# Kernel tuning notes

Hardware: AMD Instinct MI355X
Metric: run time of the kernel (lower is better)

## Reference

```python
import jax, jax.numpy as jnp
import numpy as np
from jax import lax

B, T, C = 4, 2048, 1024
E, DFF, TOPK = 8, 4096, 2


def setup_inputs() -> dict:
    key = jax.random.key(0)
    ks = jax.random.split(key, 5)
    scale = 0.02
    x = jax.random.normal(ks[0], (B, T, C), dtype=jnp.float32)
    router_w = jax.random.normal(ks[1], (C, E), dtype=jnp.float32) * scale
    router_b = jnp.zeros((E,), dtype=jnp.float32)
    w1 = jax.random.normal(ks[2], (E, C, DFF), dtype=jnp.float32) * scale
    b1 = jnp.zeros((E, DFF), dtype=jnp.float32)
    w2 = jax.random.normal(ks[3], (E, DFF, C), dtype=jnp.float32) * scale
    b2 = jnp.zeros((E, C), dtype=jnp.float32)
    return {"x": x, "router_w": router_w, "router_b": router_b,
            "w1": w1, "b1": b1, "w2": w2, "b2": b2, "top_k": TOPK}


def reference(x, router_w, router_b, w1, b1, w2, b2, top_k):
    # Router: softmax then top-k (matches torch.topk(F.softmax(logits)))
    logits = jnp.einsum('btc,ce->bte', x, router_w) + router_b   # [B,T,E]
    probs = jax.nn.softmax(logits, axis=-1)
    weights, indices = lax.top_k(probs, top_k)                    # [B,T,k]
    n_exp = w1.shape[0]
    # Combined per-expert weight per token (sum over top-k slots hitting expert j)
    onehot = jax.nn.one_hot(indices, n_exp, dtype=x.dtype)        # [B,T,k,E]
    cw = jnp.sum(weights[..., None] * onehot, axis=-2)            # [B,T,E]
    bsz, seq, dim = x.shape
    flat_x = x.reshape(-1, dim)                                   # [N,C]
    flat_cw = cw.reshape(-1, n_exp)                               # [N,E]
    out = jnp.zeros_like(flat_x)
    for j in range(n_exp):  # fixed small expert loop (dropout=0 -> eval)
        h = jax.nn.gelu(flat_x @ w1[j] + b1[j], approximate=False)
        out = out + flat_cw[:, j:j + 1] * (h @ w2[j] + b2[j])
    return out.reshape(bsz, seq, dim)
```

## Files before the change

kernel.cpp:

```cpp
#include <hip/hip_runtime.h>
#include <math.h>

typedef __bf16 bf16;
typedef bf16 bf16x4 __attribute__((ext_vector_type(4)));
typedef bf16 bf16x8 __attribute__((ext_vector_type(8)));
typedef float f32x4 __attribute__((ext_vector_type(4)));

#define NTOK 8192
#define CDIM 1024
#define EXP 8
#define DFF 4096
#define BM 128
#define BN 128
#define BK 32

__device__ __forceinline__ void gld_lds16(const bf16* g, bf16* l) {
  __builtin_amdgcn_global_load_lds(
      (const __attribute__((address_space(1))) unsigned int*)g,
      (__attribute__((address_space(3))) unsigned int*)l, 16, 0, 0);
}

__global__ __launch_bounds__(256) void convert_x(const float* __restrict__ in,
                                                 bf16* __restrict__ out) {
  int idx = (blockIdx.x * 256 + threadIdx.x) * 8;
  float4 a = *(const float4*)(in + idx);
  float4 b = *(const float4*)(in + idx + 4);
  bf16x8 v;
  v[0] = (bf16)a.x; v[1] = (bf16)a.y; v[2] = (bf16)a.z; v[3] = (bf16)a.w;
  v[4] = (bf16)b.x; v[5] = (bf16)b.y; v[6] = (bf16)b.z; v[7] = (bf16)b.w;
  *(bf16x8*)(out + idx) = v;
}

__global__ __launch_bounds__(256) void transpose_cvt(
    const float* __restrict__ in, bf16* __restrict__ out, int R, int Cin) {
  __shared__ float tile[32][33];
  int e = blockIdx.z;
  const float* ip = in + (size_t)e * R * Cin;
  bf16* op = out + (size_t)e * R * Cin;
  int c0 = blockIdx.x * 32, r0 = blockIdx.y * 32;
  int tx = threadIdx.x & 31, ty = threadIdx.x >> 5;
#pragma unroll
  for (int i = 0; i < 4; i++)
    tile[ty + 8 * i][tx] = ip[(size_t)(r0 + ty + 8 * i) * Cin + c0 + tx];
  __syncthreads();
  int c = threadIdx.x >> 3, r4 = (threadIdx.x & 7) * 4;
  bf16x4 v;
  v[0] = (bf16)tile[r4][c];
  v[1] = (bf16)tile[r4 + 1][c];
  v[2] = (bf16)tile[r4 + 2][c];
  v[3] = (bf16)tile[r4 + 3][c];
  *(bf16x4*)&op[(size_t)(c0 + c) * R + r0 + r4] = v;
}

__global__ __launch_bounds__(256) void router_kernel(
    const float* __restrict__ x, const float* __restrict__ rw,
    const float* __restrict__ rb, unsigned int* __restrict__ cnt,
    int* __restrict__ list, float* __restrict__ wq) {
  int wave = threadIdx.x >> 6, lane = threadIdx.x & 63;
  int t = blockIdx.x * 4 + wave;
  if (t >= NTOK) return;
  const float* xr = x + (size_t)t * CDIM;
  float acc[8] = {0.f, 0.f, 0.f, 0.f, 0.f, 0.f, 0.f, 0.f};
  for (int c = lane; c < CDIM; c += 64) {
    float xv = xr[c];
    const float4* rp = (const float4*)(rw + c * 8);
    float4 r0 = rp[0], r1 = rp[1];
    acc[0] += xv * r0.x; acc[1] += xv * r0.y;
    acc[2] += xv * r0.z; acc[3] += xv * r0.w;
    acc[4] += xv * r1.x; acc[5] += xv * r1.y;
    acc[6] += xv * r1.z; acc[7] += xv * r1.w;
  }
#pragma unroll
  for (int e = 0; e < 8; e++)
#pragma unroll
    for (int off = 32; off; off >>= 1) acc[e] += __shfl_down(acc[e], off);
  if (lane == 0) {
    float p[8], mx = -1e30f;
#pragma unroll
    for (int e = 0; e < 8; e++) { p[e] = acc[e] + rb[e]; mx = fmaxf(mx, p[e]); }
    float s = 0.f;
#pragma unroll
    for (int e = 0; e < 8; e++) { p[e] = expf(p[e] - mx); s += p[e]; }
    float inv = 1.0f / s;
#pragma unroll
    for (int e = 0; e < 8; e++) p[e] *= inv;
    int i1 = 0;
#pragma unroll
    for (int e = 1; e < 8; e++) if (p[e] > p[i1]) i1 = e;
    int i2 = (i1 == 0) ? 1 : 0;
#pragma unroll
    for (int e = 0; e < 8; e++) if (e != i1 && p[e] > p[i2]) i2 = e;
    unsigned s0 = atomicAdd(&cnt[i1], 1u);
    list[i1 * NTOK + s0] = t * 2;
    unsigned s1 = atomicAdd(&cnt[i2], 1u);
    list[i2 * NTOK + s1] = t * 2 + 1;
    wq[t * 2] = p[i1];
    wq[t * 2 + 1] = p[i2];
  }
}

__global__ __launch_bounds__(256) void gemm1_kernel(
    const bf16* __restrict__ xb, const bf16* __restrict__ w1b,
    const float* __restrict__ b1, const int* __restrict__ list,
    const unsigned int* __restrict__ cnt, bf16* __restrict__ h) {
  int e = blockIdx.z;
  int count = (int)min(cnt[e], (unsigned)NTOK);
  int m0 = blockIdx.y * BM;
  if (m0 >= count) return;
  int n0 = blockIdx.x * BN;

  __shared__ __align__(16) bf16 As[BM][BK];
  __shared__ __align__(16) bf16 Bs[BN][BK];
  __shared__ int Ls[BM];

  int tid = threadIdx.x;
  if (tid < BM) {
    int gi = m0 + tid;
    Ls[tid] = (gi < count) ? list[e * NTOK + gi] : 0;
  }
  __syncthreads();

  const bf16* arow0 = xb + (size_t)(Ls[tid >> 2] >> 1) * CDIM + (tid & 3) * 8;
  const bf16* arow1 =
      xb + (size_t)(Ls[64 + (tid >> 2)] >> 1) * CDIM + (tid & 3) * 8;
  bf16* adst0 = &As[tid >> 2][(tid & 3) * 8];
  bf16* adst1 = &As[64 + (tid >> 2)][(tid & 3) * 8];
  const bf16* brow0 = w1b + (size_t)e * DFF * CDIM +
                      (size_t)(n0 + (tid >> 2)) * CDIM + (tid & 3) * 8;
  const bf16* brow1 = brow0 + (size_t)64 * CDIM;
  bf16* bdst0 = &Bs[tid >> 2][(tid & 3) * 8];
  bf16* bdst1 = &Bs[64 + (tid >> 2)][(tid & 3) * 8];

  f32x4 acc[4][4] = {};
  int wave = tid >> 6, lane = tid & 63;
  int wm = wave & 1, wn = wave >> 1;
  int ln = lane & 15, kq = lane >> 4;

  for (int k0 = 0; k0 < CDIM; k0 += BK) {
    __syncthreads();
    gld_lds16(arow0 + k0, adst0);
    gld_lds16(arow1 + k0, adst1);
    gld_lds16(brow0 + k0, bdst0);
    gld_lds16(brow1 + k0, bdst1);
    __syncthreads();
    bf16x8 af[4], bfr[4];
#pragma unroll
    for (int i = 0; i < 4; i++)
      af[i] = *(bf16x8*)&As[wm * 64 + i * 16 + ln][kq * 8];
#pragma unroll
    for (int j = 0; j < 4; j++)
      bfr[j] = *(bf16x8*)&Bs[wn * 64 + j * 16 + ln][kq * 8];
#pragma unroll
    for (int i = 0; i < 4; i++)
#pragma unroll
      for (int j = 0; j < 4; j++)
        acc[i][j] = __builtin_amdgcn_mfma_f32_16x16x32_bf16(af[i], bfr[j],
                                                            acc[i][j], 0, 0, 0);
  }
#pragma unroll
  for (int j = 0; j < 4; j++) {
    int n = n0 + wn * 64 + j * 16 + ln;
    float b1v = b1[e * DFF + n];
#pragma unroll
    for (int i = 0; i < 4; i++) {
#pragma unroll
      for (int r = 0; r < 4; r++) {
        int mrow = wm * 64 + i * 16 + kq * 4 + r;
        if (m0 + mrow < count) {
          int enc = Ls[mrow];
          float v = acc[i][j][r] + b1v;
          float g = 0.5f * v * (1.0f + erff(v * 0.70710678118654752f));
          h[(size_t)enc * DFF + n] = (bf16)g;
        }
      }
    }
  }
}

__global__ __launch_bounds__(256) void gemm2_kernel(
    const bf16* __restrict__ h, const bf16* __restrict__ w2b,
    const float* __restrict__ b2, const int* __restrict__ list,
    const unsigned int* __restrict__ cnt, const float* __restrict__ wq,
    float* __restrict__ out) {
  int e = blockIdx.z;
  int count = (int)min(cnt[e], (unsigned)NTOK);
  int m0 = blockIdx.y * BM;
  if (m0 >= count) return;
  int n0 = blockIdx.x * BN;

  __shared__ __align__(16) bf16 As[BM][BK];
  __shared__ __align__(16) bf16 Bs[BN][BK];
  __shared__ int Ls[BM];

  int tid = threadIdx.x;
  if (tid < BM) {
    int gi = m0 + tid;
    Ls[tid] = (gi < count) ? list[e * NTOK + gi] : 0;
  }
  __syncthreads();

  const bf16* arow0 = h + (size_t)Ls[tid >> 2] * DFF + (tid & 3) * 8;
  const bf16* arow1 = h + (size_t)Ls[64 + (tid >> 2)] * DFF + (tid & 3) * 8;
  bf16* adst0 = &As[tid >> 2][(tid & 3) * 8];
  bf16* adst1 = &As[64 + (tid >> 2)][(tid & 3) * 8];
  const bf16* brow0 = w2b + (size_t)e * CDIM * DFF +
                      (size_t)(n0 + (tid >> 2)) * DFF + (tid & 3) * 8;
  const bf16* brow1 = brow0 + (size_t)64 * DFF;
  bf16* bdst0 = &Bs[tid >> 2][(tid & 3) * 8];
  bf16* bdst1 = &Bs[64 + (tid >> 2)][(tid & 3) * 8];

  f32x4 acc[4][4] = {};
  int wave = tid >> 6, lane = tid & 63;
  int wm = wave & 1, wn = wave >> 1;
  int ln = lane & 15, kq = lane >> 4;

  for (int k0 = 0; k0 < DFF; k0 += BK) {
    __syncthreads();
    gld_lds16(arow0 + k0, adst0);
    gld_lds16(arow1 + k0, adst1);
    gld_lds16(brow0 + k0, bdst0);
    gld_lds16(brow1 + k0, bdst1);
    __syncthreads();
    bf16x8 af[4], bfr[4];
#pragma unroll
    for (int i = 0; i < 4; i++)
      af[i] = *(bf16x8*)&As[wm * 64 + i * 16 + ln][kq * 8];
#pragma unroll
    for (int j = 0; j < 4; j++)
      bfr[j] = *(bf16x8*)&Bs[wn * 64 + j * 16 + ln][kq * 8];
#pragma unroll
    for (int i = 0; i < 4; i++)
#pragma unroll
      for (int j = 0; j < 4; j++)
        acc[i][j] = __builtin_amdgcn_mfma_f32_16x16x32_bf16(af[i], bfr[j],
                                                            acc[i][j], 0, 0, 0);
  }
#pragma unroll
  for (int j = 0; j < 4; j++) {
    int n = n0 + wn * 64 + j * 16 + ln;
    float b2v = b2[e * CDIM + n];
#pragma unroll
    for (int i = 0; i < 4; i++) {
#pragma unroll
      for (int r = 0; r < 4; r++) {
        int mrow = wm * 64 + i * 16 + kq * 4 + r;
        if (m0 + mrow < count) {
          int enc = Ls[mrow];
          int t = enc >> 1;
          float w = wq[enc];
          atomicAdd(&out[(size_t)t * CDIM + n], w * (acc[i][j][r] + b2v));
        }
      }
    }
  }
}

extern "C" void kernel_launch(void* const* d_in, const int* in_sizes, int n_in,
                              void* d_out, int out_size, void* d_ws,
                              size_t ws_size, hipStream_t stream) {
  const float* x = (const float*)d_in[0];
  const float* rw = (const float*)d_in[1];
  const float* rb = (const float*)d_in[2];
  const float* w1 = (const float*)d_in[3];
  const float* b1 = (const float*)d_in[4];
  const float* w2 = (const float*)d_in[5];
  const float* b2 = (const float*)d_in[6];
  float* out = (float*)d_out;

  char* ws = (char*)d_ws;
  size_t o = 0;
  auto carve = [&](size_t bytes) {
    void* p = ws + o;
    o = (o + bytes + 255) & ~(size_t)255;
    return p;
  };
  bf16* w1b = (bf16*)carve((size_t)EXP * DFF * CDIM * 2);
  bf16* w2b = (bf16*)carve((size_t)EXP * DFF * CDIM * 2);
  bf16* h = (bf16*)carve((size_t)2 * NTOK * DFF * 2);
  bf16* xb = (bf16*)carve((size_t)NTOK * CDIM * 2);
  int* list = (int*)carve((size_t)EXP * NTOK * 4);
  float* wq = (float*)carve((size_t)2 * NTOK * 4);
  unsigned int* cnt = (unsigned int*)carve(64);

  hipMemsetAsync(out, 0, (size_t)out_size * sizeof(float), stream);
  hipMemsetAsync(cnt, 0, 64, stream);

  convert_x<<<NTOK * CDIM / (256 * 8), 256, 0, stream>>>(x, xb);
  transpose_cvt<<<dim3(DFF / 32, CDIM / 32, EXP), 256, 0, stream>>>(w1, w1b,
                                                                    CDIM, DFF);
  transpose_cvt<<<dim3(CDIM / 32, DFF / 32, EXP), 256, 0, stream>>>(w2, w2b,
                                                                    DFF, CDIM);
  router_kernel<<<NTOK / 4, 256, 0, stream>>>(x, rw, rb, cnt, list, wq);
  gemm1_kernel<<<dim3(DFF / BN, NTOK / BM, EXP), 256, 0, stream>>>(
      xb, w1b, b1, list, cnt, h);
  gemm2_kernel<<<dim3(CDIM / BN, NTOK / BM, EXP), 256, 0, stream>>>(
      h, w2b, b2, list, cnt, wq, out);
}
```

Before: 1.175 ms.

## Enlarge MoE GEMM tiles to 256x256x64 with swizzled LDS and block remapping

Both expert GEMMs move from 128x128x32 tiles with 256 threads to 256x256x64 tiles with 512 threads, so each wave computes a 128x64 sub-tile. Operand reuse per LDS load goes up. LDS columns are XOR-swizzled on both the load and read sides to avoid bank conflicts. Workgroup IDs are remapped in groups of 8 to improve cache locality across experts and tiles. Larger tiles waste more work on partially filled expert tiles, and the bigger accumulator raises register pressure, which can limit occupancy.

```diff
diff --git a/kernel.cpp b/kernel.cpp
--- a/kernel.cpp
+++ b/kernel.cpp
@@ -10,9 +10,9 @@
 #define CDIM 1024
 #define EXP 8
 #define DFF 4096
-#define BM 128
-#define BN 128
-#define BK 32
+#define BM 256
+#define BN 256
+#define BK 64
 
 __device__ __forceinline__ void gld_lds16(const bf16* g, bf16* l) {
   __builtin_amdgcn_global_load_lds(
@@ -99,157 +99,179 @@
   }
 }
 
-__global__ __launch_bounds__(256) void gemm1_kernel(
+__global__ __launch_bounds__(512, 2) void gemm1_kernel(
     const bf16* __restrict__ xb, const bf16* __restrict__ w1b,
     const float* __restrict__ b1, const int* __restrict__ list,
     const unsigned int* __restrict__ cnt, bf16* __restrict__ h) {
-  int e = blockIdx.z;
+  int bid = blockIdx.x + 16 * (blockIdx.y + 32 * blockIdx.z);
+  int wg = (bid & 7) * 512 + (bid >> 3);
+  int n0 = (wg & 15) * BN;
+  int mt = (wg >> 4) & 31;
+  int e = wg >> 9;
   int count = (int)min(cnt[e], (unsigned)NTOK);
-  int m0 = blockIdx.y * BM;
+  int m0 = mt * BM;
   if (m0 >= count) return;
-  int n0 = blockIdx.x * BN;
 
   __shared__ __align__(16) bf16 As[BM][BK];
   __shared__ __align__(16) bf16 Bs[BN][BK];
-  __shared__ int Ls[BM];
 
   int tid = threadIdx.x;
-  if (tid < BM) {
-    int gi = m0 + tid;
-    Ls[tid] = (gi < count) ? list[e * NTOK + gi] : 0;
-  }
-  __syncthreads();
-
-  const bf16* arow0 = xb + (size_t)(Ls[tid >> 2] >> 1) * CDIM + (tid & 3) * 8;
-  const bf16* arow1 =
-      xb + (size_t)(Ls[64 + (tid >> 2)] >> 1) * CDIM + (tid & 3) * 8;
-  bf16* adst0 = &As[tid >> 2][(tid & 3) * 8];
-  bf16* adst1 = &As[64 + (tid >> 2)][(tid & 3) * 8];
-  const bf16* brow0 = w1b + (size_t)e * DFF * CDIM +
-                      (size_t)(n0 + (tid >> 2)) * CDIM + (tid & 3) * 8;
-  const bf16* brow1 = brow0 + (size_t)64 * CDIM;
-  bf16* bdst0 = &Bs[tid >> 2][(tid & 3) * 8];
-  bf16* bdst1 = &Bs[64 + (tid >> 2)][(tid & 3) * 8];
-
-  f32x4 acc[4][4] = {};
-  int wave = tid >> 6, lane = tid & 63;
-  int wm = wave & 1, wn = wave >> 1;
-  int ln = lane & 15, kq = lane >> 4;
+  int w = tid >> 6, l = tid & 63;
+  int lhi = l >> 3, llo = l & 7;
+  int w8l = w * 8 + lhi;
+  int dst8 = llo * 8;
+  int sc8 = (llo ^ lhi) * 8;
+
+  const int* lp = list + e * NTOK;
+  const bf16* aptr[4];
+  const bf16* bptr[4];
+#pragma unroll
+  for (int p = 0; p < 4; p++) {
+    int row = p * 64 + w8l;
+    int enc = lp[min(m0 + row, count - 1)];
+    aptr[p] = xb + (size_t)(enc >> 1) * CDIM + sc8;
+    bptr[p] = w1b + (size_t)e * DFF * CDIM + (size_t)(n0 + row) * CDIM + sc8;
+  }
+
+  f32x4 acc[8][4] = {};
+  int wm = w >> 2, wn = w & 3;
+  int ln = l & 15, kq = l >> 4;
+  int rx = ln & 7;
 
   for (int k0 = 0; k0 < CDIM; k0 += BK) {
     __syncthreads();
-    gld_lds16(arow0 + k0, adst0);
-    gld_lds16(arow1 + k0, adst1);
-    gld_lds16(brow0 + k0, bdst0);
-    gld_lds16(brow1 + k0, bdst1);
+#pragma unroll
+    for (int p = 0; p < 4; p++) {
+      gld_lds16(aptr[p] + k0, &As[p * 64 + w8l][dst8]);
+      gld_lds16(bptr[p] + k0, &Bs[p * 64 + w8l][dst8]);
+    }
     __syncthreads();
-    bf16x8 af[4], bfr[4];
-#pragma unroll
-    for (int i = 0; i < 4; i++)
-      af[i] = *(bf16x8*)&As[wm * 64 + i * 16 + ln][kq * 8];
-#pragma unroll
-    for (int j = 0; j < 4; j++)
-      bfr[j] = *(bf16x8*)&Bs[wn * 64 + j * 16 + ln][kq * 8];
-#pragma unroll
-    for (int i = 0; i < 4; i++)
+#pragma unroll
+    for (int hh = 0; hh < 2; hh++) {
+      int co = ((hh * 4 + kq) ^ rx) * 8;
+      bf16x8 af[8], bfr[4];
 #pragma unroll
       for (int j = 0; j < 4; j++)
-        acc[i][j] = __builtin_amdgcn_mfma_f32_16x16x32_bf16(af[i], bfr[j],
-                                                            acc[i][j], 0, 0, 0);
-  }
-#pragma unroll
-  for (int j = 0; j < 4; j++) {
-    int n = n0 + wn * 64 + j * 16 + ln;
-    float b1v = b1[e * DFF + n];
-#pragma unroll
-    for (int i = 0; i < 4; i++) {
-#pragma unroll
-      for (int r = 0; r < 4; r++) {
-        int mrow = wm * 64 + i * 16 + kq * 4 + r;
-        if (m0 + mrow < count) {
-          int enc = Ls[mrow];
-          float v = acc[i][j][r] + b1v;
+        bfr[j] = *(bf16x8*)&Bs[wn * 64 + j * 16 + ln][co];
+#pragma unroll
+      for (int i = 0; i < 8; i++)
+        af[i] = *(bf16x8*)&As[wm * 128 + i * 16 + ln][co];
+#pragma unroll
+      for (int i = 0; i < 8; i++)
+#pragma unroll
+        for (int j = 0; j < 4; j++)
+          acc[i][j] = __builtin_amdgcn_mfma_f32_16x16x32_bf16(
+              af[i], bfr[j], acc[i][j], 0, 0, 0);
+    }
+  }
+
+  float b1f[4];
+#pragma unroll
+  for (int j = 0; j < 4; j++)
+    b1f[j] = b1[e * DFF + n0 + wn * 64 + j * 16 + ln];
+#pragma unroll
+  for (int i = 0; i < 8; i++) {
+#pragma unroll
+    for (int r = 0; r < 4; r++) {
+      int mrow = wm * 128 + i * 16 + kq * 4 + r;
+      if (m0 + mrow < count) {
+        int enc = lp[m0 + mrow];
+        bf16* hr = h + (size_t)enc * DFF + n0 + wn * 64 + ln;
+#pragma unroll
+        for (int j = 0; j < 4; j++) {
+          float v = acc[i][j][r] + b1f[j];
           float g = 0.5f * v * (1.0f + erff(v * 0.70710678118654752f));
-          h[(size_t)enc * DFF + n] = (bf16)g;
+          hr[j * 16] = (bf16)g;
         }
       }
     }
   }
 }
 
-__global__ __launch_bounds__(256) void gemm2_kernel(
+__global__ __launch_bounds__(512, 2) void gemm2_kernel(
     const bf16* __restrict__ h, const bf16* __restrict__ w2b,
     const float* __restrict__ b2, const int* __restrict__ list,
     const unsigned int* __restrict__ cnt, const float* __restrict__ wq,
     float* __restrict__ out) {
-  int e = blockIdx.z;
+  int bid = blockIdx.x + 4 * (blockIdx.y + 32 * blockIdx.z);
+  int wg = (bid & 7) * 128 + (bid >> 3);
+  int n0 = (wg & 3) * BN;
+  int mt = (wg >> 2) & 31;
+  int e = wg >> 7;
   int count = (int)min(cnt[e], (unsigned)NTOK);
-  int m0 = blockIdx.y * BM;
+  int m0 = mt * BM;
   if (m0 >= count) return;
-  int n0 = blockIdx.x * BN;
 
   __shared__ __align__(16) bf16 As[BM][BK];
   __shared__ __align__(16) bf16 Bs[BN][BK];
-  __shared__ int Ls[BM];
 
   int tid = threadIdx.x;
-  if (tid < BM) {
-    int gi = m0 + tid;
-    Ls[tid] = (gi < count) ? list[e * NTOK + gi] : 0;
-  }
-  __syncthreads();
-
-  const bf16* arow0 = h + (size_t)Ls[tid >> 2] * DFF + (tid & 3) * 8;
-  const bf16* arow1 = h + (size_t)Ls[64 + (tid >> 2)] * DFF + (tid & 3) * 8;
-  bf16* adst0 = &As[tid >> 2][(tid & 3) * 8];
-  bf16* adst1 = &As[64 + (tid >> 2)][(tid & 3) * 8];
-  const bf16* brow0 = w2b + (size_t)e * CDIM * DFF +
-                      (size_t)(n0 + (tid >> 2)) * DFF + (tid & 3) * 8;
-  const bf16* brow1 = brow0 + (size_t)64 * DFF;
-  bf16* bdst0 = &Bs[tid >> 2][(tid & 3) * 8];
-  bf16* bdst1 = &Bs[64 + (tid >> 2)][(tid & 3) * 8];
-
-  f32x4 acc[4][4] = {};
-  int wave = tid >> 6, lane = tid & 63;
-  int wm = wave & 1, wn = wave >> 1;
-  int ln = lane & 15, kq = lane >> 4;
+  int w = tid >> 6, l = tid & 63;
+  int lhi = l >> 3, llo = l & 7;
+  int w8l = w * 8 + lhi;
+  int dst8 = llo * 8;
+  int sc8 = (llo ^ lhi) * 8;
+
+  const int* lp = list + e * NTOK;
+  const bf16* aptr[4];
+  const bf16* bptr[4];
+#pragma unroll
+  for (int p = 0; p < 4; p++) {
+    int row = p * 64 + w8l;
+    int enc = lp[min(m0 + row, count - 1)];
+    aptr[p] = h + (size_t)enc * DFF + sc8;
+    bptr[p] = w2b + (size_t)e * CDIM * DFF + (size_t)(n0 + row) * DFF + sc8;
+  }
+
+  f32x4 acc[8][4] = {};
+  int wm = w >> 2, wn = w & 3;
+  int ln = l & 15, kq = l >> 4;
+  int rx = ln & 7;
 
   for (int k0 = 0; k0 < DFF; k0 += BK) {
     __syncthreads();
-    gld_lds16(arow0 + k0, adst0);
-    gld_lds16(arow1 + k0, adst1);
-    gld_lds16(brow0 + k0, bdst0);
-    gld_lds16(brow1 + k0, bdst1);
+#pragma unroll
+    for (int p = 0; p < 4; p++) {
+      gld_lds16(aptr[p] + k0, &As[p * 64 + w8l][dst8]);
+      gld_lds16(bptr[p] + k0, &Bs[p * 64 + w8l][dst8]);
+    }
     __syncthreads();
-    bf16x8 af[4], bfr[4];
-#pragma unroll
-    for (int i = 0; i < 4; i++)
-      af[i] = *(bf16x8*)&As[wm * 64 + i * 16 + ln][kq * 8];
-#pragma unroll
-    for (int j = 0; j < 4; j++)
-      bfr[j] = *(bf16x8*)&Bs[wn * 64 + j * 16 + ln][kq * 8];
-#pragma unroll
-    for (int i = 0; i < 4; i++)
+#pragma unroll
+    for (int hh = 0; hh < 2; hh++) {
+      int co = ((hh * 4 + kq) ^ rx) * 8;
+      bf16x8 af[8], bfr[4];
 #pragma unroll
       for (int j = 0; j < 4; j++)
-        acc[i][j] = __builtin_amdgcn_mfma_f32_16x16x32_bf16(af[i], bfr[j],
-                                                            acc[i][j], 0, 0, 0);
-  }
-#pragma unroll
-  for (int j = 0; j < 4; j++) {
-    int n = n0 + wn * 64 + j * 16 + ln;
-    float b2v = b2[e * CDIM + n];
-#pragma unroll
-    for (int i = 0; i < 4; i++) {
-#pragma unroll
-      for (int r = 0; r < 4; r++) {
-        int mrow = wm * 64 + i * 16 + kq * 4 + r;
-        if (m0 + mrow < count) {
-          int enc = Ls[mrow];
-          int t = enc >> 1;
-          float w = wq[enc];
-          atomicAdd(&out[(size_t)t * CDIM + n], w * (acc[i][j][r] + b2v));
-        }
+        bfr[j] = *(bf16x8*)&Bs[wn * 64 + j * 16 + ln][co];
+#pragma unroll
+      for (int i = 0; i < 8; i++)
+        af[i] = *(bf16x8*)&As[wm * 128 + i * 16 + ln][co];
+#pragma unroll
+      for (int i = 0; i < 8; i++)
+#pragma unroll
+        for (int j = 0; j < 4; j++)
+          acc[i][j] = __builtin_amdgcn_mfma_f32_16x16x32_bf16(
+              af[i], bfr[j], acc[i][j], 0, 0, 0);
+    }
+  }
+
+  float b2f[4];
+#pragma unroll
+  for (int j = 0; j < 4; j++)
+    b2f[j] = b2[e * CDIM + n0 + wn * 64 + j * 16 + ln];
+#pragma unroll
+  for (int i = 0; i < 8; i++) {
+#pragma unroll
+    for (int r = 0; r < 4; r++) {
+      int mrow = wm * 128 + i * 16 + kq * 4 + r;
+      if (m0 + mrow < count) {
+        int enc = lp[m0 + mrow];
+        int t = enc >> 1;
+        float wt = wq[enc];
+        float* orow = out + (size_t)t * CDIM + n0 + wn * 64 + ln;
+#pragma unroll
+        for (int j = 0; j < 4; j++)
+          atomicAdd(&orow[j * 16], wt * (acc[i][j][r] + b2f[j]));
       }
     }
   }
@@ -291,8 +313,8 @@
   transpose_cvt<<<dim3(CDIM / 32, DFF / 32, EXP), 256, 0, stream>>>(w2, w2b,
                                                                     DFF, CDIM);
   router_kernel<<<NTOK / 4, 256, 0, stream>>>(x, rw, rb, cnt, list, wq);
-  gemm1_kernel<<<dim3(DFF / BN, NTOK / BM, EXP), 256, 0, stream>>>(
+  gemm1_kernel<<<dim3(DFF / BN, NTOK / BM, EXP), 512, 0, stream>>>(
       xb, w1b, b1, list, cnt, h);
-  gemm2_kernel<<<dim3(CDIM / BN, NTOK / BM, EXP), 256, 0, stream>>>(
+  gemm2_kernel<<<dim3(CDIM / BN, NTOK / BM, EXP), 512, 0, stream>>>(
       h, w2b, b2, list, cnt, wq, out);
 }
```

Result: slower. 1.202 ms (+2.3%).
